# Performance work log

Hardware: AMD Instinct MI355X
Metric: run time of the kernel (lower is better)

## Reference

```python
import jax, jax.numpy as jnp
import numpy as np

B, C, H, W = 4, 64, 256, 256
HEADS = 4
HID = 128  # dim * ffn_expansion_factor
EPS = 1e-5


def _ln_chan(x, w, b):
    # LayerNorm over channel axis of [b,c,h,w] (equiv to to_3d -> LN over c -> to_4d)
    mu = x.mean(1, keepdims=True)
    var = jnp.mean((x - mu) ** 2, axis=1, keepdims=True)
    return (x - mu) / jnp.sqrt(var + EPS) * w[None, :, None, None] + b[None, :, None, None]


def _ln_last(x, w, b):
    mu = x.mean(-1, keepdims=True)
    var = jnp.mean((x - mu) ** 2, axis=-1, keepdims=True)
    return (x - mu) / jnp.sqrt(var + EPS) * w + b


def _conv1(x, Wt):
    # 1x1 conv, no bias; Wt: [out,in]
    return jnp.einsum('oi,bihw->bohw', Wt, x)


def _l2norm(x):
    # torch F.normalize(dim=-1): x / max(||x||, 1e-12)
    return x / jnp.maximum(jnp.linalg.norm(x, axis=-1, keepdims=True), 1e-12)


def _dct(inp1, inp2, Wq, Wk, Wv, temp):
    # Divide_Cross_Transformer: q from inp2, k/v from inp1; channel-wise attention
    b, c, h, w = inp1.shape
    ch = c // HEADS
    hw = h * w
    q = _conv1(inp2, Wq).reshape(b, HEADS, ch, hw)
    k = _conv1(inp1, Wk).reshape(b, HEADS, ch, hw)
    v = _conv1(inp1, Wv).reshape(b, HEADS, ch, hw)
    q = _l2norm(q)
    k = _l2norm(k)
    attn = jax.nn.softmax(jnp.einsum('bhcn,bhdn->bhcd', q, k) * temp[None], axis=-1)
    return attn, v  # attn: [b,head,ch,ch], v: [b,head,ch,hw]


def _ffn(x3, w1, b1, w2, b2):
    # torch nn.GELU default = exact erf
    hdn = jax.nn.gelu(jnp.einsum('bnc,hc->bnh', x3, w1) + b1, approximate=False)
    return jnp.einsum('bnh,ch->bnc', hdn, w2) + b2


def setup_inputs() -> dict:
    key = jax.random.key(0)
    ks = jax.random.split(key, 16)
    s = 0.05

    def n(k, shape):
        return jax.random.normal(k, shape, jnp.float32) * s

    ones = jnp.ones((C,), jnp.float32)
    zeros = jnp.zeros((C,), jnp.float32)
    return {
        'image': jax.random.normal(ks[0], (B, C, H, W), jnp.float32),
        'event': jax.random.normal(ks[1], (B, C, H, W), jnp.float32),
        'Wq_c': n(ks[2], (C, C)), 'Wk_c': n(ks[3], (C, C)), 'Wv_c': n(ks[4], (C, C)),
        'temp_c': jnp.ones((HEADS, 1, 1), jnp.float32),
        'Wq_d': n(ks[5], (C, C)), 'Wk_d': n(ks[6], (C, C)), 'Wv_d': n(ks[7], (C, C)),
        'temp_d': jnp.ones((HEADS, 1, 1), jnp.float32),
        'ln_img_w': ones, 'ln_img_b': zeros,
        'ln_evt_w': ones, 'ln_evt_b': zeros,
        'ln_com_w': ones, 'ln_com_b': zeros,
        'ln_dif_w': ones, 'ln_dif_b': zeros,
        'ln1_w': ones, 'ln1_b': zeros,
        'ln2_w': ones, 'ln2_b': zeros,
        'fc1c_w': n(ks[8], (HID, C)), 'fc1c_b': jnp.zeros((HID,), jnp.float32),
        'fc2c_w': n(ks[9], (C, HID)), 'fc2c_b': jnp.zeros((C,), jnp.float32),
        'fc1d_w': n(ks[10], (HID, C)), 'fc1d_b': jnp.zeros((HID,), jnp.float32),
        'fc2d_w': n(ks[11], (C, HID)), 'fc2d_b': jnp.zeros((C,), jnp.float32),
        'proj1_w': n(ks[12], (C, C)), 'proj2_w': n(ks[13], (C, C)),
    }


def reference(image, event, Wq_c, Wk_c, Wv_c, temp_c, Wq_d, Wk_d, Wv_d, temp_d,
              ln_img_w, ln_img_b, ln_evt_w, ln_evt_b, ln_com_w, ln_com_b,
              ln_dif_w, ln_dif_b, ln1_w, ln1_b, ln2_w, ln2_b,
              fc1c_w, fc1c_b, fc2c_w, fc2c_b, fc1d_w, fc1d_b, fc2d_w, fc2d_b,
              proj1_w, proj2_w):
    b, c, h, w = image.shape
    hw = h * w
    common = image + event
    differential = image - event

    ni = _ln_chan(image, ln_img_w, ln_img_b)
    ne = _ln_chan(event, ln_evt_w, ln_evt_b)
    nc = _ln_chan(common, ln_com_w, ln_com_b)
    nd = _ln_chan(differential, ln_dif_w, ln_dif_b)

    # common branch: shared conv weights (attn_common), attn maps multiplied
    a_ic, v_ic = _dct(ni, nc, Wq_c, Wk_c, Wv_c, temp_c)
    a_ec, v_ec = _dct(ne, nc, Wq_c, Wk_c, Wv_c, temp_c)
    a_c = a_ic * a_ec
    oc = jnp.einsum('bhcd,bhdn->bhcn', a_c, v_ic + v_ec)  # same attn for both matmuls
    oc = oc.reshape(b, c, h, w)
    oc = _conv1(oc, proj1_w)
    oc3 = oc.reshape(b, c, hw).transpose(0, 2, 1)  # b (hw) c
    oc3 = oc3 + _ffn(_ln_last(oc3, ln1_w, ln1_b), fc1c_w, fc1c_b, fc2c_w, fc2c_b)
    out_common = oc3.transpose(0, 2, 1).reshape(b, c, h, w)

    # differential branch: separate attn maps, not multiplied
    a_id, v_id = _dct(ni, nd, Wq_d, Wk_d, Wv_d, temp_d)
    a_ed, v_ed = _dct(ne, nd, Wq_d, Wk_d, Wv_d, temp_d)
    od = (jnp.einsum('bhcd,bhdn->bhcn', a_id, v_id)
          + jnp.einsum('bhcd,bhdn->bhcn', a_ed, v_ed))
    od = od.reshape(b, c, h, w)
    od = _conv1(od, proj2_w)
    od3 = od.reshape(b, c, hw).transpose(0, 2, 1)
    od3 = od3 + _ffn(_ln_last(od3, ln2_w, ln2_b), fc1d_w, fc1d_b, fc2d_w, fc2d_b)
    out_differential = od3.transpose(0, 2, 1).reshape(b, c, h, w)

    return (out_common, out_differential)
```

## Files before the change

### kernel.cpp

```cpp
#include <hip/hip_runtime.h>
#include <math.h>

typedef unsigned int u32;
typedef unsigned short u16;
typedef __attribute__((ext_vector_type(8))) short short8;
typedef __attribute__((ext_vector_type(4))) float float4v;

#define NBATCH 4
#define HW 65536

#define OFF_COV 0
#define OFF_T   131072
#define OFF_M   294912
#define OFF_P   344064
#define OFF_WC  393216
#define OFF_PAR 516096
#define WS_NEED ((size_t)(OFF_PAR + 1048576) * 4)

__device__ inline float bf2f(u16 h){ return __uint_as_float(((u32)h) << 16); }
__device__ inline u16 f2bf(float x){
  u32 u = __float_as_uint(x);
  u += 0x7fffu + ((u >> 16) & 1u);
  return (u16)(u >> 16);
}
__device__ inline u32 packbf2(float a, float b){
  u32 r;
  asm("v_cvt_pk_bf16_f32 %0, %1, %2" : "=v"(r) : "v"(a), "v"(b));
  return r;
}
__device__ inline float bfu(u32 u, int hi){
  return __uint_as_float(hi ? (u & 0xffff0000u) : (u << 16));
}

__device__ inline bool detect_f32(const void* probe, int t, int* s_cnt){
  if (t == 0) *s_cnt = 0;
  __syncthreads();
  u32 w = ((const u32*)probe)[t & 255];
  u32 ex = (w >> 7) & 0xffu;
  if (!(ex >= 113u && ex <= 133u)) atomicAdd(s_cnt, 1);
  __syncthreads();
  return *s_cnt >= 128;
}

__device__ inline bool detect_f32_wide(const void* probe, int t, int* s_cnt){
  if (t == 0) *s_cnt = 0;
  __syncthreads();
  if (t < 256){
    u32 w = ((const u32*)probe)[t];
    u32 ex = (w >> 7) & 0xffu;
    if (!(ex >= 113u && ex <= 133u)) atomicAdd(s_cnt, 1);
  }
  __syncthreads();
  return *s_cnt >= 128;
}

__device__ inline void ld8(const u16* pb, const float* pf, size_t idx, bool f32, float* o){
  if (f32){
    const float4 a = *(const float4*)(pf + idx);
    const float4 b = *(const float4*)(pf + idx + 4);
    o[0]=a.x; o[1]=a.y; o[2]=a.z; o[3]=a.w; o[4]=b.x; o[5]=b.y; o[6]=b.z; o[7]=b.w;
  } else {
    uint4 r = *(const uint4*)(pb + idx);
    const u32* p = (const u32*)&r;
    #pragma unroll
    for (int j=0;j<8;j++) o[j] = bfu(p[j>>1], j&1);
  }
}

__device__ inline void ld8_issue(const u16* pb, const float* pf, size_t idx, bool f32, uint4* r2){
  if (f32){
    r2[0] = *(const uint4*)(pf + idx);
    r2[1] = *(const uint4*)(pf + idx + 4);
  } else {
    r2[0] = *(const uint4*)(pb + idx);
  }
}
__device__ inline void ld8_unpack(const uint4* r2, bool f32, float* o){
  if (f32){
    const float* q = (const float*)r2;
    #pragma unroll
    for (int j=0;j<8;j++) o[j] = q[j];
  } else {
    const u32* p = (const u32*)r2;
    #pragma unroll
    for (int j=0;j<8;j++) o[j] = bfu(p[j>>1], j&1);
  }
}

__device__ inline void softmax16(float* l){
  float m = l[0];
  #pragma unroll
  for (int i=1;i<16;i++) m = fmaxf(m, l[i]);
  float s = 0.f;
  #pragma unroll
  for (int i=0;i<16;i++){ l[i] = __expf(l[i]-m); s += l[i]; }
  float r = 1.0f/s;
  #pragma unroll
  for (int i=0;i<16;i++) l[i] *= r;
}

__global__ __launch_bounds__(256) void convert_all(
    const void* img,
    const void* t0, const void* t1, const void* t2, const void* t3,
    const void* t4, const void* t5, const void* t6, const void* t7,
    const void* t8, const void* t9, const void* t10, const void* t11,
    const void* t12, const void* t13, const void* t14, const void* t15,
    const void* t16, const void* t17, const void* t18, const void* t19,
    const void* t20, const void* t21, const void* t22, const void* t23,
    const void* t24, const void* t25, const void* t26, const void* t27,
    const void* t28, const void* t29,
    u16* __restrict__ wc, float* __restrict__ cov)
{
  __shared__ int s_cnt;
  const int t = threadIdx.x;
  const bool f32 = detect_f32(img, t, &s_cnt);
  const int id = blockIdx.x;
  if (id >= 30){
    float4 z; z.x=0.f; z.y=0.f; z.z=0.f; z.w=0.f;
    float4* c4 = (float4*)cov + (size_t)(id-30)*16384;
    for (int j = t; j < 16384; j += 256) c4[j] = z;
    return;
  }
  const int sizes[30] = {4096,4096,4096,4,4096,4096,4096,4,
                         64,64,64,64,64,64,64,64,64,64,64,64,
                         8192,128,8192,64,8192,128,8192,64,4096,4096};
  const void* srcs[30] = {t0,t1,t2,t3,t4,t5,t6,t7,t8,t9,t10,t11,t12,t13,t14,
                          t15,t16,t17,t18,t19,t20,t21,t22,t23,t24,t25,t26,t27,t28,t29};
  const void* s = srcs[id];
  const int n = sizes[id];
  u16* d = wc + (size_t)id*8192;
  for (int j = t; j < n; j += 256)
    d[j] = f32 ? f2bf(((const float*)s)[j]) : ((const u16*)s)[j];
}

__global__ __launch_bounds__(512, 4) void k1_cov(
    const void* __restrict__ img, const void* __restrict__ evt,
    const u16* __restrict__ lniw, const u16* __restrict__ lnib,
    const u16* __restrict__ lnew, const u16* __restrict__ lneb,
    const u16* __restrict__ lncw, const u16* __restrict__ lncb,
    const u16* __restrict__ lndw, const u16* __restrict__ lndb,
    float* __restrict__ cov, float* __restrict__ par, int use_par)
{
  __shared__ u16 NtL[4*64*72];
  __shared__ float spart[8][64][5];
  __shared__ float params[8][64];
  __shared__ int s_cnt;

  const int t = threadIdx.x;
  const bool f32 = detect_f32_wide(img, t, &s_cnt);
  const u16* imgb = (const u16*)img; const float* imgf = (const float*)img;
  const u16* evtb = (const u16*)evt; const float* evtf = (const float*)evt;

  const int b = blockIdx.x >> 7;
  const int P0 = (blockIdx.x & 127) * 512;
  const int ch = t >> 3, pg = t & 7;
  const int wave = t >> 6, lane = t & 63, l15 = lane & 15, quad = lane >> 4;

  float wi=bf2f(lniw[ch]), bi=bf2f(lnib[ch]);
  float we=bf2f(lnew[ch]), be=bf2f(lneb[ch]);
  float wc_=bf2f(lncw[ch]), bc_=bf2f(lncb[ch]);
  float wd_=bf2f(lndw[ch]), bd_=bf2f(lndb[ch]);

  const int va = (wave==3)?0 : (wave==7)?1 : (wave<3)?2:3;
  const int vb = (wave==0)?2 : (wave==4)?3 :
                 ((wave==2)||(wave==6)||(wave==7))?1:0;

  float4v acc[4][4];
  #pragma unroll
  for (int i=0;i<4;i++)
    #pragma unroll
    for (int j=0;j<4;j++) acc[i][j]=(float4v)0.f;

  const size_t base = (size_t)(b*64 + ch) * HW;

  for (int it = 0; it < 8; ++it){
    const int p0 = P0 + it*64;
    float A[8], B[8];
    ld8(imgb, imgf, base + p0 + pg*8, f32, A);
    ld8(evtb, evtf, base + p0 + pg*8, f32, B);

    #pragma unroll 1
    for (int jp=0;jp<4;jp++){
      float xa=A[2*jp], xb=A[2*jp+1], ea=B[2*jp], eb=B[2*jp+1];
      float s0a=xa,     s0b=xb;
      float s1a=xa*xa,  s1b=xb*xb;
      float s2a=ea,     s2b=eb;
      float s3a=ea*ea,  s3b=eb*eb;
      float s4a=xa*ea,  s4b=xb*eb;
      #pragma unroll
      for (int m=8;m<=32;m<<=1){
        s0a+=__shfl_xor(s0a,m); s0b+=__shfl_xor(s0b,m);
        s1a+=__shfl_xor(s1a,m); s1b+=__shfl_xor(s1b,m);
        s2a+=__shfl_xor(s2a,m); s2b+=__shfl_xor(s2b,m);
        s3a+=__shfl_xor(s3a,m); s3b+=__shfl_xor(s3b,m);
        s4a+=__shfl_xor(s4a,m); s4b+=__shfl_xor(s4b,m);
      }
      if ((ch&7)==0){
        int px = pg*8 + 2*jp;
        spart[wave][px][0]=s0a; spart[wave][px][1]=s1a; spart[wave][px][2]=s2a;
        spart[wave][px][3]=s3a; spart[wave][px][4]=s4a;
        spart[wave][px+1][0]=s0b; spart[wave][px+1][1]=s1b; spart[wave][px+1][2]=s2b;
        spart[wave][px+1][3]=s3b; spart[wave][px+1][4]=s4b;
      }
    }
    __syncthreads();
    if (t < 64){
      float S0=0,S1=0,S2=0,S3=0,S4=0;
      #pragma unroll
      for (int w=0;w<8;w++){
        S0+=spart[w][t][0]; S1+=spart[w][t][1]; S2+=spart[w][t][2];
        S3+=spart[w][t][3]; S4+=spart[w][t][4];
      }
      const float inv = 0.015625f;
      float mu_i=S0*inv, mu_e=S2*inv;
      float r_i = rsqrtf(fmaf(S1,inv,-mu_i*mu_i)+1e-5f);
      float r_e = rsqrtf(fmaf(S3,inv,-mu_e*mu_e)+1e-5f);
      float mu_c=mu_i+mu_e, mu_d=mu_i-mu_e;
      float r_c = rsqrtf((S1+2.f*S4+S3)*inv - mu_c*mu_c + 1e-5f);
      float r_d = rsqrtf((S1-2.f*S4+S3)*inv - mu_d*mu_d + 1e-5f);
      params[0][t]=mu_i; params[1][t]=r_i; params[2][t]=mu_e; params[3][t]=r_e;
      params[4][t]=mu_c; params[5][t]=r_c; params[6][t]=mu_d; params[7][t]=r_d;
      if (use_par){
        float4 pv; pv.x=mu_i; pv.y=r_i; pv.z=mu_e; pv.w=r_e;
        *(float4*)(par + ((size_t)b*HW + p0 + t)*4) = pv;
      }
    }
    __syncthreads();

    {
      u32 u0[4], u1[4];
      #pragma unroll
      for (int jj=0;jj<4;jj++){
        int px = pg*8 + 2*jj;
        float2 mi01 = *(const float2*)&params[0][px];
        float2 ri01 = *(const float2*)&params[1][px];
        float2 me01 = *(const float2*)&params[2][px];
        float2 re01 = *(const float2*)&params[3][px];
        u0[jj] = packbf2(fmaf((A[2*jj]-mi01.x)*ri01.x, wi, bi),
                         fmaf((A[2*jj+1]-mi01.y)*ri01.y, wi, bi));
        u1[jj] = packbf2(fmaf((B[2*jj]-me01.x)*re01.x, we, be),
                         fmaf((B[2*jj+1]-me01.y)*re01.y, we, be));
      }
      *(uint4*)&NtL[(0*64+ch)*72 + pg*8] = make_uint4(u0[0],u0[1],u0[2],u0[3]);
      *(uint4*)&NtL[(1*64+ch)*72 + pg*8] = make_uint4(u1[0],u1[1],u1[2],u1[3]);
      #pragma unroll
      for (int jj=0;jj<4;jj++){
        int px = pg*8 + 2*jj;
        float2 mc01 = *(const float2*)&params[4][px];
        float2 rc01 = *(const float2*)&params[5][px];
        float2 md01 = *(const float2*)&params[6][px];
        float2 rd01 = *(const float2*)&params[7][px];
        float xc0=A[2*jj]+B[2*jj], xc1=A[2*jj+1]+B[2*jj+1];
        float xd0=A[2*jj]-B[2*jj], xd1=A[2*jj+1]-B[2*jj+1];
        u0[jj] = packbf2(fmaf((xc0-mc01.x)*rc01.x, wc_, bc_),
                         fmaf((xc1-mc01.y)*rc01.y, wc_, bc_));
        u1[jj] = packbf2(fmaf((xd0-md01.x)*rd01.x, wd_, bd_),
                         fmaf((xd1-md01.y)*rd01.y, wd_, bd_));
      }
      *(uint4*)&NtL[(2*64+ch)*72 + pg*8] = make_uint4(u0[0],u0[1],u0[2],u0[3]);
      *(uint4*)&NtL[(3*64+ch)*72 + pg*8] = make_uint4(u1[0],u1[1],u1[2],u1[3]);
    }
    __syncthreads();

    #pragma unroll
    for (int ks=0; ks<2; ks++){
      const int off = ks*32 + quad*8;
      short8 Af[4], Bf[4];
      #pragma unroll
      for (int mi=0;mi<4;mi++){
        Af[mi] = *(const short8*)&NtL[(va*64 + mi*16 + l15)*72 + off];
        Bf[mi] = *(const short8*)&NtL[(vb*64 + mi*16 + l15)*72 + off];
      }
      #pragma unroll
      for (int mi=0;mi<4;mi++)
        #pragma unroll
        for (int nj=0;nj<4;nj++)
          acc[mi][nj] = __builtin_amdgcn_mfma_f32_16x16x32_bf16(Af[mi], Bf[nj], acc[mi][nj], 0,0,0);
    }
  }
  float* cg = cov + ((size_t)wave*NBATCH + b)*4096;
  #pragma unroll
  for (int mi=0;mi<4;mi++)
    #pragma unroll
    for (int nj=0;nj<4;nj++){
      int row0 = mi*16 + quad*4, col = nj*16 + l15;
      #pragma unroll
      for (int r=0;r<4;r++)
        atomicAdd(&cg[(row0+r)*64 + col], acc[mi][nj][r]);
    }
}

__global__ __launch_bounds__(256) void p2_fused(
    const u16* __restrict__ Wq_c, const u16* __restrict__ Wk_c,
    const u16* __restrict__ Wq_d, const u16* __restrict__ Wk_d,
    const u16* __restrict__ Wv_c, const u16* __restrict__ Wv_d,
    const u16* __restrict__ temp_c, const u16* __restrict__ temp_d,
    const u16* __restrict__ proj1, const u16* __restrict__ proj2,
    float* __restrict__ ws)
{
  __shared__ float WL[64][65];
  __shared__ float CL[64][64];
  __shared__ float rn[6][64];
  __shared__ float GLs[4][64][16];
  __shared__ float AL[3][64][16];
  const int t = threadIdx.x;
  const int b = blockIdx.x;

  const int wsel_tab[10] = {0,1,1,2,3,3,0,0,2,2};
  const int csel_tab[10] = {0,3,7,4,3,7,1,2,5,6};
  #pragma unroll 1
  for (int which=0; which<10; ++which){
    const int wsel = wsel_tab[which], csel = csel_tab[which];
    const u16* W = (wsel==0)? Wq_c : (wsel==1)? Wk_c : (wsel==2)? Wq_d : Wk_d;
    const float* Cm = ws + ((size_t)csel*NBATCH + b)*4096;
    __syncthreads();
    { int r = t>>2, c0 = (t&3)*16;
      #pragma unroll
      for (int i=0;i<16;i++) WL[r][c0+i] = bf2f(W[r*64 + c0 + i]);
      const float4* s = (const float4*)(Cm + r*64 + c0);
      float4* d = (float4*)&CL[r][c0];
      d[0]=s[0]; d[1]=s[1]; d[2]=s[2]; d[3]=s[3]; }
    __syncthreads();
    const int r = t>>2, k0 = (t&3)*16;
    float a[16];
    #pragma unroll
    for (int i=0;i<16;i++) a[i]=0.f;
    for (int m=0;m<64;m++){
      float wv = WL[r][m];
      #pragma unroll
      for (int i=0;i<16;i++) a[i] = fmaf(wv, CL[m][k0+i], a[i]);
    }
    float* o = ws + OFF_T + ((size_t)which*NBATCH + b)*4096 + r*64 + k0;
    #pragma unroll
    for (int i=0;i<16;i++) o[i] = a[i];
  }
  __syncthreads();

  const float* T = ws + OFF_T;
  {
    int s = t>>6, c = t&63;
    const float* Tp = T + ((size_t)s*NBATCH + b)*4096 + c*64;
    const u16* Wp = (s==0)? Wq_c : (s==3)? Wq_d : Wk_c;
    float acc=0;
    for (int k=0;k<64;k++) acc = fmaf(Tp[k], bf2f(Wp[c*64+k]), acc);
    rn[s][c] = 1.0f/fmaxf(sqrtf(fmaxf(acc,0.f)), 1e-12f);
    if (t < 128){
      int s2 = 4 + (t>>6);
      const float* Tp2 = T + ((size_t)s2*NBATCH + b)*4096 + c*64;
      float acc2=0;
      for (int k=0;k<64;k++) acc2 = fmaf(Tp2[k], bf2f(Wk_d[c*64+k]), acc2);
      rn[s2][c] = 1.0f/fmaxf(sqrtf(fmaxf(acc2,0.f)), 1e-12f);
    }
  }
  #pragma unroll 1
  for (int i=0;i<16;i++){
    int e = t*16 + i;
    int s = e >> 10, c = (e>>4)&63, dl = e&15, d = (c&~15)+dl;
    const float* Tp = T + ((size_t)(6+s)*NBATCH + b)*4096 + c*64;
    const u16* Wp = ((s<2)? Wk_c : Wk_d) + d*64;
    float acc=0;
    for (int j=0;j<64;j++) acc = fmaf(Tp[j], bf2f(Wp[j]), acc);
    GLs[s][c][dl] = acc;
  }
  __syncthreads();
  if (t < 192){
    int set = t>>6, c = t&63, h = c>>4, cb = c&~15;
    if (set == 0){
      float tc = bf2f(temp_c[h]);
      float rq = rn[0][c];
      float l1[16], l2[16];
      #pragma unroll
      for (int dl=0;dl<16;dl++){
        l1[dl] = GLs[0][c][dl]*rq*rn[1][cb+dl]*tc;
        l2[dl] = GLs[1][c][dl]*rq*rn[2][cb+dl]*tc;
      }
      softmax16(l1); softmax16(l2);
      #pragma unroll
      for (int dl=0;dl<16;dl++) AL[0][c][dl] = l1[dl]*l2[dl];
    } else {
      float td = bf2f(temp_d[h]);
      float rq = rn[3][c];
      int gi = (set==1)? 2 : 3;
      int rk = (set==1)? 4 : 5;
      float l[16];
      #pragma unroll
      for (int dl=0;dl<16;dl++) l[dl] = GLs[gi][c][dl]*rq*rn[rk][cb+dl]*td;
      softmax16(l);
      #pragma unroll
      for (int dl=0;dl<16;dl++) AL[set][c][dl] = l[dl];
    }
  }
  __syncthreads();
  for (int wsel=0; wsel<3; wsel++){
    const u16* Wv = (wsel==0)? Wv_c : Wv_d;
    #pragma unroll 1
    for (int i=0;i<16;i++){
      int e = t*16+i, c = e>>6, k = e&63, cb = c&~15;
      float acc=0;
      #pragma unroll
      for (int dl=0;dl<16;dl++) acc = fmaf(AL[wsel][c][dl], bf2f(Wv[(cb+dl)*64 + k]), acc);
      ws[OFF_M + ((size_t)wsel*NBATCH + b)*4096 + c*64 + k] = acc;
    }
  }
  __syncthreads();

  #pragma unroll 1
  for (int which=0; which<3; ++which){
    const u16* W = (which==0)? proj1 : proj2;
    const float* Cm = ws + OFF_M + ((size_t)which*NBATCH + b)*4096;
    __syncthreads();
    { int r = t>>2, c0 = (t&3)*16;
      #pragma unroll
      for (int i=0;i<16;i++) WL[r][c0+i] = bf2f(W[r*64 + c0 + i]);
      const float4* s = (const float4*)(Cm + r*64 + c0);
      float4* d = (float4*)&CL[r][c0];
      d[0]=s[0]; d[1]=s[1]; d[2]=s[2]; d[3]=s[3]; }
    __syncthreads();
    const int r = t>>2, k0 = (t&3)*16;
    float a[16];
    #pragma unroll
    for (int i=0;i<16;i++) a[i]=0.f;
    for (int m=0;m<64;m++){
      float wv = WL[r][m];
      #pragma unroll
      for (int i=0;i<16;i++) a[i] = fmaf(wv, CL[m][k0+i], a[i]);
    }
    float* o = ws + OFF_P + ((size_t)which*NBATCH + b)*4096 + r*64 + k0;
    #pragma unroll
    for (int i=0;i<16;i++) o[i] = a[i];
  }
}

__global__ __launch_bounds__(256, 2) void k3_fat(
    const void* __restrict__ img, const void* __restrict__ evt,
    const u16* __restrict__ lniw, const u16* __restrict__ lnib,
    const u16* __restrict__ lnew, const u16* __restrict__ lneb,
    const u16* __restrict__ ln1w, const u16* __restrict__ ln1b,
    const u16* __restrict__ ln2w, const u16* __restrict__ ln2b,
    const u16* __restrict__ fc1cw, const u16* __restrict__ fc1cb,
    const u16* __restrict__ fc2cw, const u16* __restrict__ fc2cb,
    const u16* __restrict__ fc1dw, const u16* __restrict__ fc1db,
    const u16* __restrict__ fc2dw, const u16* __restrict__ fc2db,
    const float* __restrict__ Pmat, void* __restrict__ outp,
    const float* __restrict__ par, int use_par)
{
  __shared__ __align__(16) u16 POOL[36352];
  __shared__ float spart[4][64][4];
  __shared__ float params[64][4];
  __shared__ float b1L[128];
  __shared__ float b2L[64];
  __shared__ int s_cnt;

  u16* fc1L = POOL;
  u16* fc2L = POOL + 9216;
  u16* P0L  = POOL + 17920;
  u16* P1L  = POOL + 22528;
  u16* BIG  = POOL + 27136;

  const int t = threadIdx.x;
  const bool f32 = detect_f32(img, t, &s_cnt);
  const u16* imgb = (const u16*)img; const float* imgf = (const float*)img;
  const u16* evtb = (const u16*)evt; const float* evtf = (const float*)evt;

  const int isdiff = blockIdx.x & 1;
  const int g = blockIdx.x >> 1;
  const int b = g >> 8;
  const int P0 = (g & 255) * 256;
  const size_t obase = isdiff ? (size_t)16777216 : (size_t)0;
  const int chg = t >> 3, pg = t & 7, ch0 = chg*2;
  const int wave = t >> 6, lane = t & 63, l15 = lane & 15, quad = lane >> 4;

  const u16* fc1w = isdiff ? fc1dw : fc1cw;
  const u16* fc1b = isdiff ? fc1db : fc1cb;
  const u16* fc2w = isdiff ? fc2dw : fc2cw;
  const u16* fc2b = isdiff ? fc2db : fc2cb;
  const u16* lnfw = isdiff ? ln2w : ln1w;
  const u16* lnfb = isdiff ? ln2b : ln1b;

  { int row = t >> 1, c0 = (t & 1)*32;
    const uint4* s = (const uint4*)(fc1w + row*64 + c0);
    uint4* d = (uint4*)&fc1L[row*72 + c0];
    d[0]=s[0]; d[1]=s[1]; d[2]=s[2]; d[3]=s[3]; }
  { int row = t >> 2, c0 = (t & 3)*32;
    const uint4* s = (const uint4*)(fc2w + row*128 + c0);
    uint4* d = (uint4*)&fc2L[row*136 + c0];
    d[0]=s[0]; d[1]=s[1]; d[2]=s[2]; d[3]=s[3]; }
  if (!isdiff){
    int row = t >> 2, c0 = (t & 3)*16;
    const float* s = Pmat + (size_t)b*4096 + row*64 + c0;
    u32 u[8];
    #pragma unroll
    for (int i=0;i<8;i++) u[i] = packbf2(s[2*i], s[2*i+1]);
    uint4* d = (uint4*)&P0L[row*72 + c0];
    d[0] = make_uint4(u[0],u[1],u[2],u[3]);
    d[1] = make_uint4(u[4],u[5],u[6],u[7]);
  } else {
    int row = t >> 2, c0 = (t & 3)*16;
    const float* si_ = Pmat + ((size_t)1*NBATCH + b)*4096 + row*64 + c0;
    const float* se_ = Pmat + ((size_t)2*NBATCH + b)*4096 + row*64 + c0;
    u32 u[8];
    #pragma unroll
    for (int i=0;i<8;i++) u[i] = packbf2(si_[2*i], si_[2*i+1]);
    uint4* d = (uint4*)&P0L[row*72 + c0];
    d[0] = make_uint4(u[0],u[1],u[2],u[3]); d[1] = make_uint4(u[4],u[5],u[6],u[7]);
    #pragma unroll
    for (int i=0;i<8;i++) u[i] = packbf2(se_[2*i], se_[2*i+1]);
    uint4* d2 = (uint4*)&P1L[row*72 + c0];
    d2[0] = make_uint4(u[0],u[1],u[2],u[3]); d2[1] = make_uint4(u[4],u[5],u[6],u[7]);
  }
  if (t < 128) b1L[t] = bf2f(fc1b[t]);
  if (t < 64)  b2L[t] = bf2f(fc2b[t]);

  float wi0=bf2f(lniw[ch0]), wi1=bf2f(lniw[ch0+1]);
  float we0=bf2f(lnew[ch0]), we1=bf2f(lnew[ch0+1]);
  float bi0=bf2f(lnib[ch0]), bi1=bf2f(lnib[ch0+1]);
  float be0=bf2f(lneb[ch0]), be1=bf2f(lneb[ch0+1]);
  float bs0=bi0+be0, bs1=bi1+be1;
  float w1r[4], b1r[4];
  #pragma unroll
  for (int nj=0;nj<4;nj++){ w1r[nj]=bf2f(lnfw[nj*16+l15]); b1r[nj]=bf2f(lnfb[nj*16+l15]); }

  const size_t base_i = (size_t)(b*64 + ch0)*HW;
  uint4 rA0[2], rA1[2], rB0[2], rB1[2];
  float4 PR[8];
  if (use_par){
    ld8_issue(imgb, imgf, base_i + P0 + pg*8, f32, rA0);
    ld8_issue(imgb, imgf, base_i + HW + P0 + pg*8, f32, rA1);
    ld8_issue(evtb, evtf, base_i + P0 + pg*8, f32, rB0);
    ld8_issue(evtb, evtf, base_i + HW + P0 + pg*8, f32, rB1);
    const float4* pp = (const float4*)(par + ((size_t)b*HW + P0 + pg*8)*4);
    #pragma unroll
    for (int j=0;j<8;j++) PR[j] = pp[j];
  }
  __syncthreads();

  const int STRIDE = isdiff ? 144 : 136;
  for (int it=0; it<4; ++it){
    const int p0 = P0 + it*64;
    if (use_par){
      float A0[8], A1[8], B0[8], B1[8];
      ld8_unpack(rA0, f32, A0); ld8_unpack(rA1, f32, A1);
      ld8_unpack(rB0, f32, B0); ld8_unpack(rB1, f32, B1);
      if (!isdiff){
        #pragma unroll
        for (int j=0;j<8;j++){
          float4 pr = PR[j];
          float a0=(A0[j]-pr.x)*pr.y, a1=(A1[j]-pr.x)*pr.y;
          float c0f=(B0[j]-pr.z)*pr.w, c1f=(B1[j]-pr.z)*pr.w;
          float n0 = fmaf(a0, wi0, fmaf(c0f, we0, bs0));
          float n1 = fmaf(a1, wi1, fmaf(c1f, we1, bs1));
          *(u32*)&BIG[(pg*8+j)*136 + ch0] = packbf2(n0, n1);
        }
      } else {
        #pragma unroll
        for (int j=0;j<8;j++){
          float4 pr = PR[j];
          float a0=(A0[j]-pr.x)*pr.y, a1=(A1[j]-pr.x)*pr.y;
          float c0f=(B0[j]-pr.z)*pr.w, c1f=(B1[j]-pr.z)*pr.w;
          *(u32*)&BIG[(pg*8+j)*144 + ch0]      = packbf2(fmaf(a0,wi0,bi0), fmaf(a1,wi1,bi1));
          *(u32*)&BIG[(pg*8+j)*144 + 72 + ch0] = packbf2(fmaf(c0f,we0,be0), fmaf(c1f,we1,be1));
        }
      }
    } else {
      float A0[8], A1[8], B0[8], B1[8];
      ld8(imgb, imgf, base_i + p0 + pg*8, f32, A0);
      ld8(imgb, imgf, base_i + HW + p0 + pg*8, f32, A1);
      ld8(evtb, evtf, base_i + p0 + pg*8, f32, B0);
      ld8(evtb, evtf, base_i + HW + p0 + pg*8, f32, B1);
      float si[8], sii[8], se[8], see[8];
      #pragma unroll
      for (int j=0;j<8;j++){
        float xi0=A0[j], xi1=A1[j], xe0=B0[j], xe1=B1[j];
        si[j]=xi0+xi1; sii[j]=fmaf(xi0,xi0,xi1*xi1);
        se[j]=xe0+xe1; see[j]=fmaf(xe0,xe0,xe1*xe1);
      }
      #pragma unroll
      for (int m=8;m<=32;m<<=1)
        #pragma unroll
        for (int j=0;j<8;j++){
          si[j]+=__shfl_xor(si[j],m); sii[j]+=__shfl_xor(sii[j],m);
          se[j]+=__shfl_xor(se[j],m); see[j]+=__shfl_xor(see[j],m);
        }
      if ((chg&7)==0){
        #pragma unroll
        for (int j=0;j<8;j++){
          spart[wave][pg*8+j][0]=si[j]; spart[wave][pg*8+j][1]=sii[j];
          spart[wave][pg*8+j][2]=se[j]; spart[wave][pg*8+j][3]=see[j];
        }
      }
      __syncthreads();
      if (t<64){
        float S0=0,S1=0,S2=0,S3=0;
        #pragma unroll
        for (int w=0;w<4;w++){ S0+=spart[w][t][0]; S1+=spart[w][t][1]; S2+=spart[w][t][2]; S3+=spart[w][t][3]; }
        const float inv=0.015625f;
        float mu_i=S0*inv, mu_e=S2*inv;
        float r_i=rsqrtf(fmaf(S1,inv,-mu_i*mu_i)+1e-5f);
        float r_e=rsqrtf(fmaf(S3,inv,-mu_e*mu_e)+1e-5f);
        params[t][0]=mu_i; params[t][1]=r_i; params[t][2]=mu_e; params[t][3]=r_e;
      }
      __syncthreads();
      if (!isdiff){
        #pragma unroll
        for (int j=0;j<8;j++){
          float4 pr = *(const float4*)&params[pg*8+j][0];
          float a0=(A0[j]-pr.x)*pr.y, a1=(A1[j]-pr.x)*pr.y;
          float c0f=(B0[j]-pr.z)*pr.w, c1f=(B1[j]-pr.z)*pr.w;
          float n0 = fmaf(a0, wi0, fmaf(c0f, we0, bs0));
          float n1 = fmaf(a1, wi1, fmaf(c1f, we1, bs1));
          *(u32*)&BIG[(pg*8+j)*136 + ch0] = packbf2(n0, n1);
        }
      } else {
        #pragma unroll
        for (int j=0;j<8;j++){
          float4 pr = *(const float4*)&params[pg*8+j][0];
          float a0=(A0[j]-pr.x)*pr.y, a1=(A1[j]-pr.x)*pr.y;
          float c0f=(B0[j]-pr.z)*pr.w, c1f=(B1[j]-pr.z)*pr.w;
          *(u32*)&BIG[(pg*8+j)*144 + ch0]      = packbf2(fmaf(a0,wi0,bi0), fmaf(a1,wi1,bi1));
          *(u32*)&BIG[(pg*8+j)*144 + 72 + ch0] = packbf2(fmaf(c0f,we0,be0), fmaf(c1f,we1,be1));
        }
      }
    }
    __syncthreads();
    if (use_par && it < 3){
      const int pn = p0 + 64;
      ld8_issue(imgb, imgf, base_i + pn + pg*8, f32, rA0);
      ld8_issue(imgb, imgf, base_i + HW + pn + pg*8, f32, rA1);
      ld8_issue(evtb, evtf, base_i + pn + pg*8, f32, rB0);
      ld8_issue(evtb, evtf, base_i + HW + pn + pg*8, f32, rB1);
      const float4* pp = (const float4*)(par + ((size_t)b*HW + pn + pg*8)*4);
      #pragma unroll
      for (int j=0;j<8;j++) PR[j] = pp[j];
    }
    float4v acc1[4];
    #pragma unroll
    for (int nj=0;nj<4;nj++) acc1[nj]=(float4v)0.f;
    const int px_row = wave*16 + l15;
    if (!isdiff){
      #pragma unroll
      for (int ks=0;ks<2;ks++){
        const int off = ks*32 + quad*8;
        short8 af = *(const short8*)&BIG[px_row*136 + off];
        #pragma unroll
        for (int nj=0;nj<4;nj++){
          short8 bw = *(const short8*)&P0L[(nj*16+l15)*72 + off];
          acc1[nj] = __builtin_amdgcn_mfma_f32_16x16x32_bf16(af, bw, acc1[nj], 0,0,0);
        }
      }
    } else {
      #pragma unroll
      for (int ks=0;ks<2;ks++){
        const int off = ks*32 + quad*8;
        short8 ai = *(const short8*)&BIG[px_row*144 + off];
        short8 ae = *(const short8*)&BIG[px_row*144 + 72 + off];
        #pragma unroll
        for (int nj=0;nj<4;nj++){
          short8 bwi = *(const short8*)&P0L[(nj*16+l15)*72 + off];
          acc1[nj] = __builtin_amdgcn_mfma_f32_16x16x32_bf16(ai, bwi, acc1[nj], 0,0,0);
          short8 bwe = *(const short8*)&P1L[(nj*16+l15)*72 + off];
          acc1[nj] = __builtin_amdgcn_mfma_f32_16x16x32_bf16(ae, bwe, acc1[nj], 0,0,0);
        }
      }
    }
    float s[4], sq[4];
    #pragma unroll
    for (int j=0;j<4;j++){
      s[j] = acc1[0][j]+acc1[1][j]+acc1[2][j]+acc1[3][j];
      sq[j] = acc1[0][j]*acc1[0][j];
      sq[j] = fmaf(acc1[1][j],acc1[1][j],sq[j]);
      sq[j] = fmaf(acc1[2][j],acc1[2][j],sq[j]);
      sq[j] = fmaf(acc1[3][j],acc1[3][j],sq[j]);
    }
    #pragma unroll
    for (int m=1;m<=8;m<<=1)
      #pragma unroll
      for (int j=0;j<4;j++){ s[j]+=__shfl_xor(s[j],m); sq[j]+=__shfl_xor(sq[j],m); }
    float muj[4], rj[4];
    #pragma unroll
    for (int j=0;j<4;j++){
      muj[j]=s[j]*0.015625f;
      rj[j]=rsqrtf(fmaf(sq[j],0.015625f,-muj[j]*muj[j])+1e-5f);
    }
    #pragma unroll
    for (int nj=0;nj<4;nj++)
      #pragma unroll
      for (int j=0;j<4;j++){
        float tv = (acc1[nj][j]-muj[j])*rj[j];
        tv = fmaf(tv, w1r[nj], b1r[nj]);
        BIG[(wave*16+quad*4+j)*STRIDE + nj*16+l15] = f2bf(tv);
      }
    float4v accF[8];
    #pragma unroll
    for (int nh=0;nh<8;nh++) accF[nh]=(float4v)0.f;
    #pragma unroll
    for (int ks=0;ks<2;ks++){
      const int off = ks*32+quad*8;
      short8 af = *(const short8*)&BIG[px_row*STRIDE + off];
      #pragma unroll
      for (int nh=0;nh<8;nh++){
        short8 bw = *(const short8*)&fc1L[(nh*16+l15)*72 + off];
        accF[nh] = __builtin_amdgcn_mfma_f32_16x16x32_bf16(af, bw, accF[nh], 0,0,0);
      }
    }
    #pragma unroll
    for (int nh=0;nh<8;nh++){
      float bb = b1L[nh*16+l15];
      #pragma unroll
      for (int j=0;j<4;j++){
        float v = accF[nh][j] + bb;
        float g2 = 0.5f*v*(1.0f + erff(v*0.70710678118654752f));
        BIG[(wave*16+quad*4+j)*STRIDE + nh*16+l15] = f2bf(g2);
      }
    }
    float4v accO[4];
    #pragma unroll
    for (int nj=0;nj<4;nj++) accO[nj]=(float4v)0.f;
    #pragma unroll
    for (int ks=0;ks<4;ks++){
      const int off = ks*32+quad*8;
      short8 ag = *(const short8*)&BIG[px_row*STRIDE + off];
      #pragma unroll
      for (int nj=0;nj<4;nj++){
        short8 bw = *(const short8*)&fc2L[(nj*16+l15)*136 + off];
        accO[nj] = __builtin_amdgcn_mfma_f32_16x16x32_bf16(ag, bw, accO[nj], 0,0,0);
      }
    }
    const int px0 = p0 + wave*16 + quad*4;
    #pragma unroll
    for (int nj=0;nj<4;nj++){
      float bb = b2L[nj*16+l15];
      int r = nj*16+l15;
      float v0 = acc1[nj][0] + accO[nj][0] + bb;
      float v1 = acc1[nj][1] + accO[nj][1] + bb;
      float v2 = acc1[nj][2] + accO[nj][2] + bb;
      float v3 = acc1[nj][3] + accO[nj][3] + bb;
      size_t oi = obase + (size_t)(b*64 + r)*HW + px0;
      if (f32){ float4 fv; fv.x=v0; fv.y=v1; fv.z=v2; fv.w=v3;
        *(float4*)((float*)outp + oi) = fv; }
      else *(uint2*)((u16*)outp + oi) = make_uint2(packbf2(v0,v1), packbf2(v2,v3));
    }
    __syncthreads();
  }
}

extern "C" void kernel_launch(void* const* d_in, const int* in_sizes, int n_in,
                              void* d_out, int out_size, void* d_ws, size_t ws_size,
                              hipStream_t stream)
{
  const void* img = d_in[0];
  const void* evt = d_in[1];
  float* ws = (float*)d_ws;
  u16* wc = (u16*)(ws + OFF_WC);
  float* par = ws + OFF_PAR;
  const int use_par = (ws_size >= WS_NEED) ? 1 : 0;
  #define SLOT(i) (wc + (size_t)((i)-2)*8192)

  convert_all<<<dim3(32), dim3(256), 0, stream>>>(img,
      d_in[2], d_in[3], d_in[4], d_in[5], d_in[6], d_in[7], d_in[8], d_in[9],
      d_in[10], d_in[11], d_in[12], d_in[13], d_in[14], d_in[15], d_in[16], d_in[17],
      d_in[18], d_in[19], d_in[20], d_in[21], d_in[22], d_in[23], d_in[24], d_in[25],
      d_in[26], d_in[27], d_in[28], d_in[29], d_in[30], d_in[31], wc, ws);
  k1_cov<<<dim3(512), dim3(512), 0, stream>>>(img, evt,
      SLOT(10), SLOT(11), SLOT(12), SLOT(13), SLOT(14), SLOT(15), SLOT(16), SLOT(17),
      ws, par, use_par);
  p2_fused<<<dim3(4), dim3(256), 0, stream>>>(
      SLOT(2), SLOT(3), SLOT(6), SLOT(7), SLOT(4), SLOT(8), SLOT(5), SLOT(9),
      SLOT(30), SLOT(31), ws);
  k3_fat<<<dim3(2048), dim3(256), 0, stream>>>(img, evt,
      SLOT(10), SLOT(11), SLOT(12), SLOT(13),
      SLOT(18), SLOT(19), SLOT(20), SLOT(21),
      SLOT(22), SLOT(23), SLOT(24), SLOT(25),
      SLOT(26), SLOT(27), SLOT(28), SLOT(29),
      ws + OFF_P, d_out, par, use_par);
  #undef SLOT
}
```

Baseline: 605.7 us.

## Split small-matrix stage into parallel kernels and specialize FFN tail per branch

The single 4-block p2_fused kernel becomes three launches: p2a runs the ten 64x64 weight-by-covariance products across 40 blocks, p2b does the norms and softmax per batch, and p2c runs the projections across 12 blocks. This spreads a serial, nearly single-CU stage over more compute units, at the cost of two extra kernel launches. The main kernel now takes a compile-time LDS stride through a templated tail, one instance per branch, and remaps block indices so that groups of 8 blocks share the same branch.

Result: faster. 560.1 us (-7.5%).

```diff
diff --git a/kernel.cpp b/kernel.cpp
--- a/kernel.cpp
+++ b/kernel.cpp
@@ -290,52 +290,63 @@
     }
 }
 
-__global__ __launch_bounds__(256) void p2_fused(
+__global__ __launch_bounds__(256) void p2a(
     const u16* __restrict__ Wq_c, const u16* __restrict__ Wk_c,
     const u16* __restrict__ Wq_d, const u16* __restrict__ Wk_d,
-    const u16* __restrict__ Wv_c, const u16* __restrict__ Wv_d,
-    const u16* __restrict__ temp_c, const u16* __restrict__ temp_d,
-    const u16* __restrict__ proj1, const u16* __restrict__ proj2,
     float* __restrict__ ws)
 {
   __shared__ float WL[64][65];
   __shared__ float CL[64][64];
+  const int t = threadIdx.x;
+  const int b = blockIdx.x & 3;
+  const int which = blockIdx.x >> 2;
+  int wsel, csel;
+  switch (which){
+    case 0: wsel=0; csel=0; break;
+    case 1: wsel=1; csel=3; break;
+    case 2: wsel=1; csel=7; break;
+    case 3: wsel=2; csel=4; break;
+    case 4: wsel=3; csel=3; break;
+    case 5: wsel=3; csel=7; break;
+    case 6: wsel=0; csel=1; break;
+    case 7: wsel=0; csel=2; break;
+    case 8: wsel=2; csel=5; break;
+    default: wsel=2; csel=6; break;
+  }
+  const u16* W = (wsel==0)? Wq_c : (wsel==1)? Wk_c : (wsel==2)? Wq_d : Wk_d;
+  const float* Cm = ws + ((size_t)csel*NBATCH + b)*4096;
+  { int r = t>>2, c0 = (t&3)*16;
+    #pragma unroll
+    for (int i=0;i<16;i++) WL[r][c0+i] = bf2f(W[r*64 + c0 + i]);
+    const float4* s = (const float4*)(Cm + r*64 + c0);
+    float4* d = (float4*)&CL[r][c0];
+    d[0]=s[0]; d[1]=s[1]; d[2]=s[2]; d[3]=s[3]; }
+  __syncthreads();
+  const int r = t>>2, k0 = (t&3)*16;
+  float a[16];
+  #pragma unroll
+  for (int i=0;i<16;i++) a[i]=0.f;
+  for (int m=0;m<64;m++){
+    float wv = WL[r][m];
+    #pragma unroll
+    for (int i=0;i<16;i++) a[i] = fmaf(wv, CL[m][k0+i], a[i]);
+  }
+  float* o = ws + OFF_T + ((size_t)which*NBATCH + b)*4096 + r*64 + k0;
+  #pragma unroll
+  for (int i=0;i<16;i++) o[i] = a[i];
+}
+
+__global__ __launch_bounds__(256) void p2b(
+    float* __restrict__ ws,
+    const u16* __restrict__ Wq_c, const u16* __restrict__ Wk_c,
+    const u16* __restrict__ Wq_d, const u16* __restrict__ Wk_d,
+    const u16* __restrict__ Wv_c, const u16* __restrict__ Wv_d,
+    const u16* __restrict__ temp_c, const u16* __restrict__ temp_d)
+{
+  const int b = blockIdx.x, t = threadIdx.x;
   __shared__ float rn[6][64];
   __shared__ float GLs[4][64][16];
   __shared__ float AL[3][64][16];
-  const int t = threadIdx.x;
-  const int b = blockIdx.x;
-
-  const int wsel_tab[10] = {0,1,1,2,3,3,0,0,2,2};
-  const int csel_tab[10] = {0,3,7,4,3,7,1,2,5,6};
-  #pragma unroll 1
-  for (int which=0; which<10; ++which){
-    const int wsel = wsel_tab[which], csel = csel_tab[which];
-    const u16* W = (wsel==0)? Wq_c : (wsel==1)? Wk_c : (wsel==2)? Wq_d : Wk_d;
-    const float* Cm = ws + ((size_t)csel*NBATCH + b)*4096;
-    __syncthreads();
-    { int r = t>>2, c0 = (t&3)*16;
-      #pragma unroll
-      for (int i=0;i<16;i++) WL[r][c0+i] = bf2f(W[r*64 + c0 + i]);
-      const float4* s = (const float4*)(Cm + r*64 + c0);
-      float4* d = (float4*)&CL[r][c0];
-      d[0]=s[0]; d[1]=s[1]; d[2]=s[2]; d[3]=s[3]; }
-    __syncthreads();
-    const int r = t>>2, k0 = (t&3)*16;
-    float a[16];
-    #pragma unroll
-    for (int i=0;i<16;i++) a[i]=0.f;
-    for (int m=0;m<64;m++){
-      float wv = WL[r][m];
-      #pragma unroll
-      for (int i=0;i<16;i++) a[i] = fmaf(wv, CL[m][k0+i], a[i]);
-    }
-    float* o = ws + OFF_T + ((size_t)which*NBATCH + b)*4096 + r*64 + k0;
-    #pragma unroll
-    for (int i=0;i<16;i++) o[i] = a[i];
-  }
-  __syncthreads();
-
   const float* T = ws + OFF_T;
   {
     int s = t>>6, c = t&63;
@@ -402,36 +413,127 @@
       ws[OFF_M + ((size_t)wsel*NBATCH + b)*4096 + c*64 + k] = acc;
     }
   }
+}
+
+__global__ __launch_bounds__(256) void p2c(
+    const u16* __restrict__ proj1, const u16* __restrict__ proj2,
+    float* __restrict__ ws)
+{
+  __shared__ float WL[64][65];
+  __shared__ float CL[64][64];
+  const int t = threadIdx.x;
+  const int b = blockIdx.x & 3;
+  const int which = blockIdx.x >> 2;
+  const u16* W = (which==0)? proj1 : proj2;
+  const float* Cm = ws + OFF_M + ((size_t)which*NBATCH + b)*4096;
+  { int r = t>>2, c0 = (t&3)*16;
+    #pragma unroll
+    for (int i=0;i<16;i++) WL[r][c0+i] = bf2f(W[r*64 + c0 + i]);
+    const float4* s = (const float4*)(Cm + r*64 + c0);
+    float4* d = (float4*)&CL[r][c0];
+    d[0]=s[0]; d[1]=s[1]; d[2]=s[2]; d[3]=s[3]; }
   __syncthreads();
-
-  #pragma unroll 1
-  for (int which=0; which<3; ++which){
-    const u16* W = (which==0)? proj1 : proj2;
-    const float* Cm = ws + OFF_M + ((size_t)which*NBATCH + b)*4096;
-    __syncthreads();
-    { int r = t>>2, c0 = (t&3)*16;
-      #pragma unroll
-      for (int i=0;i<16;i++) WL[r][c0+i] = bf2f(W[r*64 + c0 + i]);
-      const float4* s = (const float4*)(Cm + r*64 + c0);
-      float4* d = (float4*)&CL[r][c0];
-      d[0]=s[0]; d[1]=s[1]; d[2]=s[2]; d[3]=s[3]; }
-    __syncthreads();
-    const int r = t>>2, k0 = (t&3)*16;
-    float a[16];
-    #pragma unroll
-    for (int i=0;i<16;i++) a[i]=0.f;
-    for (int m=0;m<64;m++){
-      float wv = WL[r][m];
-      #pragma unroll
-      for (int i=0;i<16;i++) a[i] = fmaf(wv, CL[m][k0+i], a[i]);
-    }
-    float* o = ws + OFF_P + ((size_t)which*NBATCH + b)*4096 + r*64 + k0;
-    #pragma unroll
-    for (int i=0;i<16;i++) o[i] = a[i];
-  }
-}
-
-__global__ __launch_bounds__(256, 2) void k3_fat(
+  const int r = t>>2, k0 = (t&3)*16;
+  float a[16];
+  #pragma unroll
+  for (int i=0;i<16;i++) a[i]=0.f;
+  for (int m=0;m<64;m++){
+    float wv = WL[r][m];
+    #pragma unroll
+    for (int i=0;i<16;i++) a[i] = fmaf(wv, CL[m][k0+i], a[i]);
+  }
+  float* o = ws + OFF_P + ((size_t)which*NBATCH + b)*4096 + r*64 + k0;
+  #pragma unroll
+  for (int i=0;i<16;i++) o[i] = a[i];
+}
+
+template<int STRIDE>
+__device__ inline void k3_tail(
+    u16* __restrict__ BIG, const u16* __restrict__ fc1L, const u16* __restrict__ fc2L,
+    const float* __restrict__ b1L, const float* __restrict__ b2L,
+    float4v* acc1, const float* w1r, const float* b1r,
+    int wave, int quad, int l15, int px_row,
+    void* __restrict__ outp, size_t obase, int b, int px0, bool f32)
+{
+  float s[4], sq[4];
+  #pragma unroll
+  for (int j=0;j<4;j++){
+    s[j] = acc1[0][j]+acc1[1][j]+acc1[2][j]+acc1[3][j];
+    sq[j] = acc1[0][j]*acc1[0][j];
+    sq[j] = fmaf(acc1[1][j],acc1[1][j],sq[j]);
+    sq[j] = fmaf(acc1[2][j],acc1[2][j],sq[j]);
+    sq[j] = fmaf(acc1[3][j],acc1[3][j],sq[j]);
+  }
+  #pragma unroll
+  for (int m=1;m<=8;m<<=1)
+    #pragma unroll
+    for (int j=0;j<4;j++){ s[j]+=__shfl_xor(s[j],m); sq[j]+=__shfl_xor(sq[j],m); }
+  float muj[4], rj[4];
+  #pragma unroll
+  for (int j=0;j<4;j++){
+    muj[j]=s[j]*0.015625f;
+    rj[j]=rsqrtf(fmaf(sq[j],0.015625f,-muj[j]*muj[j])+1e-5f);
+  }
+  #pragma unroll
+  for (int nj=0;nj<4;nj++)
+    #pragma unroll
+    for (int j=0;j<4;j++){
+      float tv = (acc1[nj][j]-muj[j])*rj[j];
+      tv = fmaf(tv, w1r[nj], b1r[nj]);
+      BIG[(wave*16+quad*4+j)*STRIDE + nj*16+l15] = f2bf(tv);
+    }
+  float4v accF[8];
+  #pragma unroll
+  for (int nh=0;nh<8;nh++) accF[nh]=(float4v)0.f;
+  #pragma unroll
+  for (int ks=0;ks<2;ks++){
+    const int off = ks*32+quad*8;
+    short8 af = *(const short8*)&BIG[px_row*STRIDE + off];
+    #pragma unroll
+    for (int nh=0;nh<8;nh++){
+      short8 bw = *(const short8*)&fc1L[(nh*16+l15)*72 + off];
+      accF[nh] = __builtin_amdgcn_mfma_f32_16x16x32_bf16(af, bw, accF[nh], 0,0,0);
+    }
+  }
+  #pragma unroll
+  for (int nh=0;nh<8;nh++){
+    float bb = b1L[nh*16+l15];
+    #pragma unroll
+    for (int j=0;j<4;j++){
+      float v = accF[nh][j] + bb;
+      float g2 = 0.5f*v*(1.0f + erff(v*0.70710678118654752f));
+      BIG[(wave*16+quad*4+j)*STRIDE + nh*16+l15] = f2bf(g2);
+    }
+  }
+  float4v accO[4];
+  #pragma unroll
+  for (int nj=0;nj<4;nj++) accO[nj]=(float4v)0.f;
+  #pragma unroll
+  for (int ks=0;ks<4;ks++){
+    const int off = ks*32+quad*8;
+    short8 ag = *(const short8*)&BIG[px_row*STRIDE + off];
+    #pragma unroll
+    for (int nj=0;nj<4;nj++){
+      short8 bw = *(const short8*)&fc2L[(nj*16+l15)*136 + off];
+      accO[nj] = __builtin_amdgcn_mfma_f32_16x16x32_bf16(ag, bw, accO[nj], 0,0,0);
+    }
+  }
+  #pragma unroll
+  for (int nj=0;nj<4;nj++){
+    float bb = b2L[nj*16+l15];
+    int r = nj*16+l15;
+    float v0 = acc1[nj][0] + accO[nj][0] + bb;
+    float v1 = acc1[nj][1] + accO[nj][1] + bb;
+    float v2 = acc1[nj][2] + accO[nj][2] + bb;
+    float v3 = acc1[nj][3] + accO[nj][3] + bb;
+    size_t oi = obase + (size_t)(b*64 + r)*HW + px0;
+    if (f32){ float4 fv; fv.x=v0; fv.y=v1; fv.z=v2; fv.w=v3;
+      *(float4*)((float*)outp + oi) = fv; }
+    else *(uint2*)((u16*)outp + oi) = make_uint2(packbf2(v0,v1), packbf2(v2,v3));
+  }
+}
+
+__global__ __launch_bounds__(256, 2) void k3_fat2(
     const void* __restrict__ img, const void* __restrict__ evt,
     const u16* __restrict__ lniw, const u16* __restrict__ lnib,
     const u16* __restrict__ lnew, const u16* __restrict__ lneb,
@@ -462,10 +564,11 @@
   const u16* imgb = (const u16*)img; const float* imgf = (const float*)img;
   const u16* evtb = (const u16*)evt; const float* evtf = (const float*)evt;
 
-  const int isdiff = blockIdx.x & 1;
-  const int g = blockIdx.x >> 1;
-  const int b = g >> 8;
-  const int P0 = (g & 255) * 256;
+  const int bid = blockIdx.x;
+  const int isdiff = (bid >> 3) & 1;
+  const int slab = (bid & 7) | ((bid >> 4) << 3);
+  const int b = slab >> 8;
+  const int P0 = (slab & 255) * 256;
   const size_t obase = isdiff ? (size_t)16777216 : (size_t)0;
   const int chg = t >> 3, pg = t & 7, ch0 = chg*2;
   const int wave = t >> 6, lane = t & 63, l15 = lane & 15, quad = lane >> 4;
@@ -534,7 +637,6 @@
   }
   __syncthreads();
 
-  const int STRIDE = isdiff ? 144 : 136;
   for (int it=0; it<4; ++it){
     const int p0 = P0 + it*64;
     if (use_par){
@@ -636,6 +738,7 @@
     #pragma unroll
     for (int nj=0;nj<4;nj++) acc1[nj]=(float4v)0.f;
     const int px_row = wave*16 + l15;
+    const int px0 = p0 + wave*16 + quad*4;
     if (!isdiff){
       #pragma unroll
       for (int ks=0;ks<2;ks++){
@@ -647,6 +750,8 @@
           acc1[nj] = __builtin_amdgcn_mfma_f32_16x16x32_bf16(af, bw, acc1[nj], 0,0,0);
         }
       }
+      k3_tail<136>(BIG, fc1L, fc2L, b1L, b2L, acc1, w1r, b1r,
+                   wave, quad, l15, px_row, outp, obase, b, px0, f32);
     } else {
       #pragma unroll
       for (int ks=0;ks<2;ks++){
@@ -661,83 +766,8 @@
           acc1[nj] = __builtin_amdgcn_mfma_f32_16x16x32_bf16(ae, bwe, acc1[nj], 0,0,0);
         }
       }
-    }
-    float s[4], sq[4];
-    #pragma unroll
-    for (int j=0;j<4;j++){
-      s[j] = acc1[0][j]+acc1[1][j]+acc1[2][j]+acc1[3][j];
-      sq[j] = acc1[0][j]*acc1[0][j];
-      sq[j] = fmaf(acc1[1][j],acc1[1][j],sq[j]);
-      sq[j] = fmaf(acc1[2][j],acc1[2][j],sq[j]);
-      sq[j] = fmaf(acc1[3][j],acc1[3][j],sq[j]);
-    }
-    #pragma unroll
-    for (int m=1;m<=8;m<<=1)
-      #pragma unroll
-      for (int j=0;j<4;j++){ s[j]+=__shfl_xor(s[j],m); sq[j]+=__shfl_xor(sq[j],m); }
-    float muj[4], rj[4];
-    #pragma unroll
-    for (int j=0;j<4;j++){
-      muj[j]=s[j]*0.015625f;
-      rj[j]=rsqrtf(fmaf(sq[j],0.015625f,-muj[j]*muj[j])+1e-5f);
-    }
-    #pragma unroll
-    for (int nj=0;nj<4;nj++)
-      #pragma unroll
-      for (int j=0;j<4;j++){
-        float tv = (acc1[nj][j]-muj[j])*rj[j];
-        tv = fmaf(tv, w1r[nj], b1r[nj]);
-        BIG[(wave*16+quad*4+j)*STRIDE + nj*16+l15] = f2bf(tv);
-      }
-    float4v accF[8];
-    #pragma unroll
-    for (int nh=0;nh<8;nh++) accF[nh]=(float4v)0.f;
-    #pragma unroll
-    for (int ks=0;ks<2;ks++){
-      const int off = ks*32+quad*8;
-      short8 af = *(const short8*)&BIG[px_row*STRIDE + off];
-      #pragma unroll
-      for (int nh=0;nh<8;nh++){
-        short8 bw = *(const short8*)&fc1L[(nh*16+l15)*72 + off];
-        accF[nh] = __builtin_amdgcn_mfma_f32_16x16x32_bf16(af, bw, accF[nh], 0,0,0);
-      }
-    }
-    #pragma unroll
-    for (int nh=0;nh<8;nh++){
-      float bb = b1L[nh*16+l15];
-      #pragma unroll
-      for (int j=0;j<4;j++){
-        float v = accF[nh][j] + bb;
-        float g2 = 0.5f*v*(1.0f + erff(v*0.70710678118654752f));
-        BIG[(wave*16+quad*4+j)*STRIDE + nh*16+l15] = f2bf(g2);
-      }
-    }
-    float4v accO[4];
-    #pragma unroll
-    for (int nj=0;nj<4;nj++) accO[nj]=(float4v)0.f;
-    #pragma unroll
-    for (int ks=0;ks<4;ks++){
-      const int off = ks*32+quad*8;
-      short8 ag = *(const short8*)&BIG[px_row*STRIDE + off];
-      #pragma unroll
-      for (int nj=0;nj<4;nj++){
-        short8 bw = *(const short8*)&fc2L[(nj*16+l15)*136 + off];
-        accO[nj] = __builtin_amdgcn_mfma_f32_16x16x32_bf16(ag, bw, accO[nj], 0,0,0);
-      }
-    }
-    const int px0 = p0 + wave*16 + quad*4;
-    #pragma unroll
-    for (int nj=0;nj<4;nj++){
-      float bb = b2L[nj*16+l15];
-      int r = nj*16+l15;
-      float v0 = acc1[nj][0] + accO[nj][0] + bb;
-      float v1 = acc1[nj][1] + accO[nj][1] + bb;
-      float v2 = acc1[nj][2] + accO[nj][2] + bb;
-      float v3 = acc1[nj][3] + accO[nj][3] + bb;
-      size_t oi = obase + (size_t)(b*64 + r)*HW + px0;
-      if (f32){ float4 fv; fv.x=v0; fv.y=v1; fv.z=v2; fv.w=v3;
-        *(float4*)((float*)outp + oi) = fv; }
-      else *(uint2*)((u16*)outp + oi) = make_uint2(packbf2(v0,v1), packbf2(v2,v3));
+      k3_tail<144>(BIG, fc1L, fc2L, b1L, b2L, acc1, w1r, b1r,
+                   wave, quad, l15, px_row, outp, obase, b, px0, f32);
     }
     __syncthreads();
   }
@@ -763,10 +793,11 @@
   k1_cov<<<dim3(512), dim3(512), 0, stream>>>(img, evt,
       SLOT(10), SLOT(11), SLOT(12), SLOT(13), SLOT(14), SLOT(15), SLOT(16), SLOT(17),
       ws, par, use_par);
-  p2_fused<<<dim3(4), dim3(256), 0, stream>>>(
-      SLOT(2), SLOT(3), SLOT(6), SLOT(7), SLOT(4), SLOT(8), SLOT(5), SLOT(9),
-      SLOT(30), SLOT(31), ws);
-  k3_fat<<<dim3(2048), dim3(256), 0, stream>>>(img, evt,
+  p2a<<<dim3(40), dim3(256), 0, stream>>>(SLOT(2), SLOT(3), SLOT(6), SLOT(7), ws);
+  p2b<<<dim3(4), dim3(256), 0, stream>>>(ws, SLOT(2), SLOT(3), SLOT(6), SLOT(7),
+      SLOT(4), SLOT(8), SLOT(5), SLOT(9));
+  p2c<<<dim3(12), dim3(256), 0, stream>>>(SLOT(30), SLOT(31), ws);
+  k3_fat2<<<dim3(2048), dim3(256), 0, stream>>>(img, evt,
       SLOT(10), SLOT(11), SLOT(12), SLOT(13),
       SLOT(18), SLOT(19), SLOT(20), SLOT(21),
       SLOT(22), SLOT(23), SLOT(24), SLOT(25),
```
